# Performance work log

Hardware: AMD Instinct MI355X
Metric: run time of the kernel (lower is better)

## Reference

```python
import jax, jax.numpy as jnp
import numpy as np

B, H, W, C, NH, WS, SS = 16, 112, 112, 384, 12, 7, 3
HD = C // NH          # head dim = 32
N = WS * WS           # tokens per window = 49
MLP_H = 4 * C         # 1536
NW = (H // WS) * (W // WS)  # windows per image = 256


def _rel_pos_index():
    coords = np.stack(np.meshgrid(np.arange(WS), np.arange(WS), indexing='ij')).reshape(2, -1)
    rel = (coords[:, :, None] - coords[:, None, :]).transpose(1, 2, 0)  # (N, N, 2)
    rel[..., 0] += WS - 1
    rel[..., 1] += WS - 1
    rel[..., 0] *= 2 * WS - 1
    return rel.sum(-1)  # (N, N) in [0, (2WS-1)^2)


def _attn_mask():
    img = np.zeros((H, W))
    cnt = 0
    slices = (slice(0, -WS), slice(-WS, -SS), slice(-SS, None))
    for hs in slices:
        for ws_ in slices:
            img[hs, ws_] = cnt
            cnt += 1
    mw = img.reshape(H // WS, WS, W // WS, WS).transpose(0, 2, 1, 3).reshape(-1, N)
    am = mw[:, None, :] - mw[:, :, None]
    return np.where(am != 0, -100.0, 0.0).astype(np.float32)  # (NW, N, N)


REL_IDX = jnp.asarray(_rel_pos_index().reshape(-1))  # (N*N,) int
MASK = jnp.asarray(_attn_mask())                      # (NW, N, N)


def _ln(x, g, b, eps=1e-5):
    m = jnp.mean(x, -1, keepdims=True)
    v = jnp.mean((x - m) ** 2, -1, keepdims=True)
    return (x - m) / jnp.sqrt(v + eps) * g + b


def setup_inputs() -> dict:
    key = jax.random.key(0)
    ks = jax.random.split(key, 16)
    s = 0.02
    return {
        'x': jax.random.normal(ks[0], (B, H * W, C), jnp.float32),
        'norm1_g': jnp.ones((C,), jnp.float32),
        'norm1_b': jnp.zeros((C,), jnp.float32),
        'qkv_w': jax.random.normal(ks[1], (C, 3 * C), jnp.float32) * s,
        'qkv_b': jnp.zeros((3 * C,), jnp.float32),
        'proj_w': jax.random.normal(ks[2], (C, C), jnp.float32) * s,
        'proj_b': jnp.zeros((C,), jnp.float32),
        'rpb_table': jax.random.normal(ks[3], ((2 * WS - 1) ** 2, NH), jnp.float32) * s,
        'norm2_g': jnp.ones((C,), jnp.float32),
        'norm2_b': jnp.zeros((C,), jnp.float32),
        'fc1_w': jax.random.normal(ks[4], (C, MLP_H), jnp.float32) * s,
        'fc1_b': jnp.zeros((MLP_H,), jnp.float32),
        'fc2_w': jax.random.normal(ks[5], (MLP_H, C), jnp.float32) * s,
        'fc2_b': jnp.zeros((C,), jnp.float32),
    }


def reference(x, norm1_g, norm1_b, qkv_w, qkv_b, proj_w, proj_b, rpb_table,
              norm2_g, norm2_b, fc1_w, fc1_b, fc2_w, fc2_b):
    shortcut = x
    h = _ln(x, norm1_g, norm1_b).reshape(B, H, W, C)
    # cyclic shift
    h = jnp.roll(h, (-SS, -SS), axis=(1, 2))
    # window partition -> (B*NW, N, C)
    wins = h.reshape(B, H // WS, WS, W // WS, WS, C).transpose(0, 1, 3, 2, 4, 5).reshape(-1, N, C)
    qkv = (wins @ qkv_w + qkv_b).reshape(-1, N, 3, NH, HD).transpose(2, 0, 3, 1, 4)
    q, k, v = qkv[0] * HD ** -0.5, qkv[1], qkv[2]  # (B*NW, NH, N, HD)
    attn = jnp.einsum('bhnd,bhmd->bhnm', q, k)
    bias = rpb_table[REL_IDX].reshape(N, N, NH).transpose(2, 0, 1)  # (NH, N, N)
    attn = attn + bias[None]
    attn = (attn.reshape(B, NW, NH, N, N) + MASK[None, :, None]).reshape(-1, NH, N, N)
    attn = jax.nn.softmax(attn, axis=-1)
    out = jnp.einsum('bhnm,bhmd->bhnd', attn, v).transpose(0, 2, 1, 3).reshape(-1, N, C)
    out = out @ proj_w + proj_b
    # window reverse
    out = out.reshape(B, H // WS, W // WS, WS, WS, C).transpose(0, 1, 3, 2, 4, 5).reshape(B, H, W, C)
    out = jnp.roll(out, (SS, SS), axis=(1, 2)).reshape(B, H * W, C)
    x = shortcut + out
    h2 = _ln(x, norm2_g, norm2_b)
    h2 = jax.nn.gelu(h2 @ fc1_w + fc1_b, approximate=False) @ fc2_w + fc2_b
    return x + h2
```

## Files before the change

### kernel.cpp

```cpp
#include <hip/hip_runtime.h>
#include <hip/hip_bf16.h>

typedef short bf16x8 __attribute__((ext_vector_type(8)));
typedef float f32x4 __attribute__((ext_vector_type(4)));
typedef float f32x16 __attribute__((ext_vector_type(16)));
typedef unsigned int u32x4 __attribute__((ext_vector_type(4)));

typedef __attribute__((address_space(1))) void gvoid;
typedef __attribute__((address_space(3))) void lvoid;

__device__ __forceinline__ short f2b(float f) {
  __hip_bfloat16 h = __float2bfloat16(f);
  return __builtin_bit_cast(short, h);
}

__device__ __forceinline__ f32x4 mfma16(bf16x8 a, bf16x8 b, f32x4 c) {
  return __builtin_amdgcn_mfma_f32_16x16x32_bf16(a, b, c, 0, 0, 0);
}

__device__ __forceinline__ f32x16 mfma32(bf16x8 a, bf16x8 b, f32x16 c) {
  return __builtin_amdgcn_mfma_f32_32x32x16_bf16(a, b, c, 0, 0, 0);
}

__device__ __forceinline__ unsigned cvtpk(float lo, float hi) {
  unsigned r;
  asm("v_cvt_pk_bf16_f32 %0, %1, %2" : "=v"(r) : "v"(lo), "v"(hi));
  return r;
}

__device__ __forceinline__ void gload16(const void* g, void* l) {
  __builtin_amdgcn_global_load_lds((const gvoid*)g, (lvoid*)l, 16, 0, 0);
}

__global__ __launch_bounds__(256) void convT_k(const float* __restrict__ src,
                                               short* __restrict__ dst, int K,
                                               int N, int scale_cols,
                                               float scale) {
  int idx = blockIdx.x * 256 + threadIdx.x;
  if (idx >= N * K) return;
  int n = idx / K, k = idx % K;
  float v = src[(size_t)k * N + n];
  if (n < scale_cols) v *= scale;
  dst[idx] = f2b(v);
}

__global__ __launch_bounds__(256) void scale_bias_k(const float* __restrict__ src,
                                                    float* __restrict__ dst,
                                                    int n, int scale_cols,
                                                    float scale) {
  int i = blockIdx.x * 256 + threadIdx.x;
  if (i >= n) return;
  dst[i] = src[i] * (i < scale_cols ? scale : 1.f);
}

__global__ __launch_bounds__(256) void biasmask_k(const float* __restrict__ rpb,
                                                  float* __restrict__ tbl) {
  int idx = blockIdx.x * 256 + threadIdx.x;
  int q = idx & 63, key = (idx >> 6) & 63;
  int hc = idx >> 12;
  int h = hc % 12, cls = hc / 12;
  float v;
  if (q >= 49 || key >= 49) {
    v = -1e4f;
  } else {
    int i1 = q / 7, j1 = q % 7, i2 = key / 7, j2 = key % 7;
    v = rpb[(size_t)((i1 - i2 + 6) * 13 + (j1 - j2 + 6)) * 12 + h];
    int clsh = cls >> 1, clsw = cls & 1;
    int rq = (clsh ? 1 + (i1 >= 4) : 0) * 3 + (clsw ? 1 + (j1 >= 4) : 0);
    int rk = (clsh ? 1 + (i2 >= 4) : 0) * 3 + (clsw ? 1 + (j2 >= 4) : 0);
    if (rq != rk) v -= 100.f;
  }
  tbl[idx] = v;
}

template <bool GATHER>
__device__ __forceinline__ void ln_body(const float* __restrict__ x,
                                        const float* __restrict__ gw,
                                        const float* __restrict__ bw,
                                        short* __restrict__ out) {
  const int lane = threadIdx.x & 63;
  const int t = (blockIdx.x << 2) + (threadIdx.x >> 6);
  size_t srow;
  if (GATHER) {
    int bb = t / 12544, rm2 = t % 12544;
    int wi = rm2 / 49, nn = rm2 % 49;
    int wh = wi >> 4, ww = wi & 15;
    int ii = nn / 7, jj = nn % 7;
    int rr = wh * 7 + ii + 3; if (rr >= 112) rr -= 112;
    int cc = ww * 7 + jj + 3; if (cc >= 112) cc -= 112;
    srow = ((size_t)bb * 12544 + rr * 112 + cc) * 384;
  } else {
    srow = (size_t)t * 384;
  }
  const float2* src = (const float2*)(x + srow);
  const float2* g2 = (const float2*)gw;
  const float2* b2 = (const float2*)bw;
  float2 u[3];
  float s = 0.f, ss = 0.f;
#pragma unroll
  for (int k = 0; k < 3; ++k) {
    u[k] = src[lane + (k << 6)];
    s += u[k].x + u[k].y;
    ss += u[k].x * u[k].x + u[k].y * u[k].y;
  }
#pragma unroll
  for (int m = 1; m < 64; m <<= 1) {
    s += __shfl_xor(s, m, 64);
    ss += __shfl_xor(ss, m, 64);
  }
  const float mean = s * (1.f / 384.f);
  const float var = ss * (1.f / 384.f) - mean * mean;
  const float rstd = rsqrtf(var + 1e-5f);
  unsigned* o = (unsigned*)(out + (size_t)t * 384);
#pragma unroll
  for (int k = 0; k < 3; ++k) {
    int c = lane + (k << 6);
    float2 gv = g2[c], bv = b2[c];
    unsigned lo = (unsigned short)f2b((u[k].x - mean) * rstd * gv.x + bv.x);
    unsigned hi = (unsigned short)f2b((u[k].y - mean) * rstd * gv.y + bv.y);
    o[c] = lo | (hi << 16);
  }
}

__global__ __launch_bounds__(256) void ln1_k(const float* __restrict__ x,
                                             const float* __restrict__ gw,
                                             const float* __restrict__ bw,
                                             short* __restrict__ out) {
  ln_body<true>(x, gw, bw, out);
}
__global__ __launch_bounds__(256) void ln2_k(const float* __restrict__ x,
                                             const float* __restrict__ gw,
                                             const float* __restrict__ bw,
                                             short* __restrict__ out) {
  ln_body<false>(x, gw, bw, out);
}

template <int EPI>
__device__ __forceinline__ void gemm_body(
    const short* __restrict__ A, int lda, const short* __restrict__ BT,
    int ldb, const float* __restrict__ bias, int K, short* __restrict__ outh,
    int ldo, float* __restrict__ outf, const float* __restrict__ resid) {
  __shared__ __align__(16) short A0s[8192], B0s[8192];
  __shared__ __align__(16) short A1s[8192], B1s[8192];
  const int tid = threadIdx.x;
  const int gx = gridDim.x;
  int lin = blockIdx.y * gx + blockIdx.x;
  const int cpx = (gx * gridDim.y) >> 3;
  lin = (lin & 7) * cpx + (lin >> 3);
  const int m0 = (lin / gx) << 7, n0 = (lin % gx) << 7;
  const int lane = tid & 63;
  const int wave = tid >> 6;
  const int wr = (wave >> 1) << 6, wc = (wave & 1) << 6;
  const int g = lane >> 4, q = lane & 15;
  const int q7 = q & 7;
  const int rd0 = ((g) ^ q7) << 3;
  const int rd1 = ((4 + g) ^ q7) << 3;
  const int cswz = ((tid & 7) ^ ((tid >> 3) & 7)) << 3;
  const int ldst = tid << 3;

  f32x4 acc[4][4];
#pragma unroll
  for (int i = 0; i < 4; ++i)
#pragma unroll
    for (int j = 0; j < 4; ++j) acc[i][j] = (f32x4){0.f, 0.f, 0.f, 0.f};

  const short* Abase = A + (size_t)(m0 + (tid >> 3)) * lda + cswz;
  const short* Bbase = BT + (size_t)(n0 + (tid >> 3)) * ldb + cswz;

#define STAGE(kt, DA, DB)                                                     \
  do {                                                                        \
    _Pragma("unroll") for (int p = 0; p < 4; ++p) {                           \
      gload16(Abase + (size_t)(32 * p) * lda + (kt), &DA[2048 * p + ldst]);   \
      gload16(Bbase + (size_t)(32 * p) * ldb + (kt), &DB[2048 * p + ldst]);   \
    }                                                                         \
  } while (0)

#define COMPUTE(SA, SB)                                                       \
  do {                                                                        \
    _Pragma("unroll") for (int kk = 0; kk < 2; ++kk) {                        \
      const int rdo = kk ? rd1 : rd0;                                         \
      bf16x8 af[4], bfv[4];                                                   \
      _Pragma("unroll") for (int mi = 0; mi < 4; ++mi)                        \
          af[mi] = *(const bf16x8*)&SA[(wr + mi * 16 + q) * 64 + rdo];        \
      _Pragma("unroll") for (int ni = 0; ni < 4; ++ni)                        \
          bfv[ni] = *(const bf16x8*)&SB[(wc + ni * 16 + q) * 64 + rdo];       \
      _Pragma("unroll") for (int mi = 0; mi < 4; ++mi)                        \
          _Pragma("unroll") for (int ni = 0; ni < 4; ++ni)                    \
              acc[mi][ni] = mfma16(af[mi], bfv[ni], acc[mi][ni]);             \
    }                                                                         \
  } while (0)

  const int nt = K >> 6;
  STAGE(0, A0s, B0s);
  __syncthreads();
  for (int t = 0; t < nt; t += 2) {
    STAGE((t + 1) << 6, A1s, B1s);
    COMPUTE(A0s, B0s);
    __syncthreads();
    if (t + 2 < nt) STAGE((t + 2) << 6, A0s, B0s);
    COMPUTE(A1s, B1s);
    __syncthreads();
  }
#undef STAGE
#undef COMPUTE

  float bv[4];
#pragma unroll
  for (int ni = 0; ni < 4; ++ni)
    bv[ni] = bias ? bias[n0 + wc + ni * 16 + q] : 0.f;

#pragma unroll
  for (int mi = 0; mi < 4; ++mi) {
#pragma unroll
    for (int r = 0; r < 4; ++r) {
      const int grow = m0 + wr + mi * 16 + g * 4 + r;
      size_t orow;
      if constexpr (EPI == 2) {
        int bb = grow / 12544, rm2 = grow % 12544;
        int wi = rm2 / 49, nn = rm2 % 49;
        int wh = wi >> 4, ww = wi & 15;
        int ii = nn / 7, jj = nn % 7;
        int rr = wh * 7 + ii + 3; if (rr >= 112) rr -= 112;
        int cc = ww * 7 + jj + 3; if (cc >= 112) cc -= 112;
        orow = ((size_t)bb * 12544 + rr * 112 + cc) * 384;
      } else {
        orow = (size_t)grow * (size_t)ldo;
      }
#pragma unroll
      for (int ni = 0; ni < 4; ++ni) {
        const int gcol = n0 + wc + ni * 16 + q;
        float v = acc[mi][ni][r] + bv[ni];
        if constexpr (EPI == 0) {
          outh[orow + gcol] = f2b(v);
        } else if constexpr (EPI == 1) {
          v = 0.5f * v * (1.f + erff(v * 0.70710678118f));
          outh[orow + gcol] = f2b(v);
        } else if constexpr (EPI == 2) {
          outf[orow + gcol] = resid[orow + gcol] + v;
        } else {
          outf[orow + gcol] += v;
        }
      }
    }
  }
}

#define GEMM_WRAP(NAME, EPI)                                                   \
  __global__ __launch_bounds__(256) void NAME(                                 \
      const short* __restrict__ A, int lda, const short* __restrict__ BT,      \
      int ldb, const float* __restrict__ bias, int K,                          \
      short* __restrict__ outh, int ldo, float* __restrict__ outf,             \
      const float* __restrict__ resid) {                                       \
    gemm_body<EPI>(A, lda, BT, ldb, bias, K, outh, ldo, outf, resid);          \
  }
GEMM_WRAP(gemm_qkv_k, 0)
GEMM_WRAP(gemm_fc1_k, 1)
GEMM_WRAP(gemm_proj_k, 2)
GEMM_WRAP(gemm_fc2_k, 3)

__global__ __launch_bounds__(256) void attn_k(const short* __restrict__ qkv,
                                              const float* __restrict__ tbl,
                                              short* __restrict__ out) {
  const int lane = threadIdx.x & 63;
  const int task = blockIdx.x * 4 + (threadIdx.x >> 6);
  const int win = task / 12;
  const int h = task - win * 12;
  const int wh = (win >> 4) & 15, ww = win & 15;
  const int cls = ((wh == 15) ? 2 : 0) + ((ww == 15) ? 1 : 0);
  const int l31 = lane & 31, h5 = lane >> 5;
  const size_t tokbase = (size_t)win * 49;
  const short* base = qkv + tokbase * 1152 + h * 32;
  const bf16x8 zero8 = {0, 0, 0, 0, 0, 0, 0, 0};

  bf16x8 kf[2][2];
#pragma unroll
  for (int mi = 0; mi < 2; ++mi) {
    int row = l31 + 32 * mi;
#pragma unroll
    for (int s = 0; s < 2; ++s)
      kf[mi][s] = (row < 49)
                      ? *(const bf16x8*)(base + (size_t)row * 1152 + 384 +
                                         16 * s + 8 * h5)
                      : zero8;
  }
  bf16x8 vf[4];
#pragma unroll
  for (int kt = 0; kt < 4; ++kt) {
#pragma unroll
    for (int e = 0; e < 8; ++e) {
      int key = 16 * kt + 8 * h5 + e;
      vf[kt][e] = (key < 49) ? base[(size_t)key * 1152 + 768 + l31] : (short)0;
    }
  }

  const float* tb = tbl + ((size_t)(cls * 12 + h) << 12);

#pragma unroll
  for (int ni = 0; ni < 2; ++ni) {
    bf16x8 qf[2];
    int qrow = l31 + 32 * ni;
#pragma unroll
    for (int s = 0; s < 2; ++s)
      qf[s] = (qrow < 49)
                  ? *(const bf16x8*)(base + (size_t)qrow * 1152 + 16 * s +
                                     8 * h5)
                  : zero8;
    f32x16 st[2];
#pragma unroll
    for (int mi = 0; mi < 2; ++mi) {
      st[mi] = mfma32(kf[mi][0], qf[0], (f32x16)(0.f));
      st[mi] = mfma32(kf[mi][1], qf[1], st[mi]);
    }
#pragma unroll
    for (int mi = 0; mi < 2; ++mi)
#pragma unroll
      for (int r = 0; r < 16; ++r) {
        int koff = (r & 3) + 8 * (r >> 2) + 4 * h5;
        st[mi][r] += tb[(size_t)(32 * mi + koff) * 64 + 32 * ni + l31];
      }
    float mx = st[0][0];
#pragma unroll
    for (int r = 1; r < 16; ++r) mx = fmaxf(mx, st[0][r]);
#pragma unroll
    for (int r = 0; r < 16; ++r) mx = fmaxf(mx, st[1][r]);
    mx = fmaxf(mx, __shfl_xor(mx, 32, 64));
    float sm = 0.f;
#pragma unroll
    for (int mi = 0; mi < 2; ++mi)
#pragma unroll
      for (int r = 0; r < 16; ++r) {
        float e = __expf(st[mi][r] - mx);
        st[mi][r] = e;
        sm += e;
      }
    sm += __shfl_xor(sm, 32, 64);
    const float rinv = 1.f / sm;
#pragma unroll
    for (int mi = 0; mi < 2; ++mi)
#pragma unroll
      for (int r = 0; r < 16; ++r) st[mi][r] *= rinv;

    f32x16 acc = (f32x16)(0.f);
#pragma unroll
    for (int kt = 0; kt < 4; ++kt) {
      const int mi = kt >> 1, b8 = (kt & 1) * 8;
      unsigned q0l = cvtpk(st[mi][b8 + 0], st[mi][b8 + 1]);
      unsigned q0h = cvtpk(st[mi][b8 + 2], st[mi][b8 + 3]);
      unsigned q1l = cvtpk(st[mi][b8 + 4], st[mi][b8 + 5]);
      unsigned q1h = cvtpk(st[mi][b8 + 6], st[mi][b8 + 7]);
      unsigned sl = h5 ? q0l : q1l, sh = h5 ? q0h : q1h;
      unsigned kl = h5 ? q1l : q0l, kh = h5 ? q1h : q0h;
      unsigned rl = (unsigned)__shfl_xor((int)sl, 32, 64);
      unsigned rh = (unsigned)__shfl_xor((int)sh, 32, 64);
      u32x4 fr;
      fr[0] = h5 ? rl : kl;
      fr[1] = h5 ? rh : kh;
      fr[2] = h5 ? kl : rl;
      fr[3] = h5 ? kh : rh;
      acc = mfma32(__builtin_bit_cast(bf16x8, fr), vf[kt], acc);
    }
#pragma unroll
    for (int r = 0; r < 16; ++r) {
      int query = 32 * ni + (r & 3) + 8 * (r >> 2) + 4 * h5;
      if (ni == 0 || query < 49)
        out[(tokbase + query) * 384 + h * 32 + l31] = f2b(acc[r]);
    }
  }
}

extern "C" void kernel_launch(void* const* d_in, const int* in_sizes, int n_in,
                              void* d_out, int out_size, void* d_ws,
                              size_t ws_size, hipStream_t stream) {
  const float* x = (const float*)d_in[0];
  const float* n1g = (const float*)d_in[1];
  const float* n1b = (const float*)d_in[2];
  const float* qkvw = (const float*)d_in[3];
  const float* qkvb = (const float*)d_in[4];
  const float* projw = (const float*)d_in[5];
  const float* projb = (const float*)d_in[6];
  const float* rpb = (const float*)d_in[7];
  const float* n2g = (const float*)d_in[8];
  const float* n2b = (const float*)d_in[9];
  const float* fc1w = (const float*)d_in[10];
  const float* fc1b = (const float*)d_in[11];
  const float* fc2w = (const float*)d_in[12];
  const float* fc2b = (const float*)d_in[13];
  float* out = (float*)d_out;

  char* ws = (char*)d_ws;
  short* w_qkvT = (short*)(ws + 0);
  short* w_projT = (short*)(ws + 884736);
  short* w_fc1T = (short*)(ws + 1179648);
  short* w_fc2T = (short*)(ws + 2359296);
  float* w_qb = (float*)(ws + 3538944);
  float* tbl = (float*)(ws + 3543552);
  const size_t o_qkv = 4329984;
  short* qkvbuf = (short*)(ws + o_qkv);
  const size_t o_hwin = o_qkv + 462422016ull;
  short* hwin = (short*)(ws + o_hwin);
  const size_t o_fc1 = o_hwin + 154140672ull;

  int NC;
  size_t fc1_off = o_fc1;
  if (ws_size >= o_fc1 + 616562688ull) NC = 1;
  else if (ws_size >= o_fc1 + 308281344ull) NC = 2;
  else if (ws_size >= o_fc1 + 154140672ull) NC = 4;
  else { NC = 4; fc1_off = o_hwin; }
  short* fc1c = (short*)(ws + fc1_off);
  short* h2 = qkvbuf;

  const float qscale = 0.17677669529663687f;

  convT_k<<<(442368 + 255) / 256, 256, 0, stream>>>(qkvw, w_qkvT, 384, 1152, 384, qscale);
  convT_k<<<(147456 + 255) / 256, 256, 0, stream>>>(projw, w_projT, 384, 384, 0, 1.f);
  convT_k<<<(589824 + 255) / 256, 256, 0, stream>>>(fc1w, w_fc1T, 384, 1536, 0, 1.f);
  convT_k<<<(589824 + 255) / 256, 256, 0, stream>>>(fc2w, w_fc2T, 1536, 384, 0, 1.f);
  scale_bias_k<<<5, 256, 0, stream>>>(qkvb, w_qb, 1152, 384, qscale);
  biasmask_k<<<768, 256, 0, stream>>>(rpb, tbl);

  ln1_k<<<50176, 256, 0, stream>>>(x, n1g, n1b, hwin);
  gemm_qkv_k<<<dim3(9, 1568), 256, 0, stream>>>(hwin, 384, w_qkvT, 384, w_qb,
                                                384, qkvbuf, 1152, nullptr,
                                                nullptr);
  attn_k<<<12288, 256, 0, stream>>>(qkvbuf, tbl, hwin);
  gemm_proj_k<<<dim3(3, 1568), 256, 0, stream>>>(hwin, 384, w_projT, 384,
                                                 projb, 384, nullptr, 384, out,
                                                 x);
  ln2_k<<<50176, 256, 0, stream>>>(out, n2g, n2b, h2);
  const int CK = 1536 / NC;
  for (int c = 0; c < NC; ++c) {
    gemm_fc1_k<<<dim3(CK >> 7, 1568), 256, 0, stream>>>(
        h2, 384, w_fc1T + (size_t)c * CK * 384, 384, fc1b + c * CK, 384, fc1c,
        CK, nullptr, nullptr);
    gemm_fc2_k<<<dim3(3, 1568), 256, 0, stream>>>(
        fc1c, CK, w_fc2T + c * CK, 1536, (c == 0) ? fc2b : nullptr, CK,
        nullptr, 384, out, nullptr);
  }
}
```

Baseline: 2.128 ms.

## Interleave GEMM global-to-LDS loads with quadrant MFMA phases

Restructures the bf16 GEMM main loop into four quadrant MFMA phases per K-tile. Global-to-LDS loads for the next tile are split into halves and interleaved between the phases, with explicit vmcnt waits, raw s_barriers, and s_setprio raised around the MFMA bursts. The goal is to overlap memory traffic with matrix math and cut full-barrier stalls. This adds more barriers and hand-tuned wait counts, and the A01 load for tile t+2 is issued into the current buffer after its reads, so correctness depends on exact ordering.

```diff
diff --git a/kernel.cpp b/kernel.cpp
--- a/kernel.cpp
+++ b/kernel.cpp
@@ -167,42 +167,106 @@
   const short* Abase = A + (size_t)(m0 + (tid >> 3)) * lda + cswz;
   const short* Bbase = BT + (size_t)(n0 + (tid >> 3)) * ldb + cswz;
 
-#define STAGE(kt, DA, DB)                                                     \
-  do {                                                                        \
-    _Pragma("unroll") for (int p = 0; p < 4; ++p) {                           \
-      gload16(Abase + (size_t)(32 * p) * lda + (kt), &DA[2048 * p + ldst]);   \
-      gload16(Bbase + (size_t)(32 * p) * ldb + (kt), &DB[2048 * p + ldst]);   \
-    }                                                                         \
-  } while (0)
-
-#define COMPUTE(SA, SB)                                                       \
-  do {                                                                        \
-    _Pragma("unroll") for (int kk = 0; kk < 2; ++kk) {                        \
-      const int rdo = kk ? rd1 : rd0;                                         \
-      bf16x8 af[4], bfv[4];                                                   \
-      _Pragma("unroll") for (int mi = 0; mi < 4; ++mi)                        \
-          af[mi] = *(const bf16x8*)&SA[(wr + mi * 16 + q) * 64 + rdo];        \
-      _Pragma("unroll") for (int ni = 0; ni < 4; ++ni)                        \
-          bfv[ni] = *(const bf16x8*)&SB[(wc + ni * 16 + q) * 64 + rdo];       \
-      _Pragma("unroll") for (int mi = 0; mi < 4; ++mi)                        \
-          _Pragma("unroll") for (int ni = 0; ni < 4; ++ni)                    \
-              acc[mi][ni] = mfma16(af[mi], bfv[ni], acc[mi][ni]);             \
-    }                                                                         \
-  } while (0)
-
+#define SA01(kt, DA)                                            \
+  do {                                                          \
+    gload16(Abase + (kt), &DA[ldst]);                           \
+    gload16(Abase + (size_t)32 * lda + (kt), &DA[2048 + ldst]); \
+  } while (0)
+#define SA23(kt, DA)                                            \
+  do {                                                          \
+    gload16(Abase + (size_t)64 * lda + (kt), &DA[4096 + ldst]); \
+    gload16(Abase + (size_t)96 * lda + (kt), &DA[6144 + ldst]); \
+  } while (0)
+#define SB01(kt, DB)                                            \
+  do {                                                          \
+    gload16(Bbase + (kt), &DB[ldst]);                           \
+    gload16(Bbase + (size_t)32 * ldb + (kt), &DB[2048 + ldst]); \
+  } while (0)
+#define SB23(kt, DB)                                            \
+  do {                                                          \
+    gload16(Bbase + (size_t)64 * ldb + (kt), &DB[4096 + ldst]); \
+    gload16(Bbase + (size_t)96 * ldb + (kt), &DB[6144 + ldst]); \
+  } while (0)
+
+#define READ_AF(i, SA)                                               \
+  do {                                                               \
+    af[i][0] = *(const bf16x8*)&SA[(wr + (i)*16 + q) * 64 + rd0];    \
+    af[i][1] = *(const bf16x8*)&SA[(wr + (i)*16 + q) * 64 + rd1];    \
+  } while (0)
+#define READ_BF(i, SB)                                               \
+  do {                                                               \
+    bfr[i][0] = *(const bf16x8*)&SB[(wc + (i)*16 + q) * 64 + rd0];   \
+    bfr[i][1] = *(const bf16x8*)&SB[(wc + (i)*16 + q) * 64 + rd1];   \
+  } while (0)
+
+#define QUAD(a, b)                                                       \
+  do {                                                                   \
+    __builtin_amdgcn_s_setprio(1);                                       \
+    _Pragma("unroll") for (int ks = 0; ks < 2; ++ks)                     \
+        _Pragma("unroll") for (int i = 0; i < 2; ++i)                    \
+            _Pragma("unroll") for (int j = 0; j < 2; ++j)                \
+                acc[2 * (a) + i][2 * (b) + j] = mfma16(                  \
+                    af[2 * (a) + i][ks], bfr[2 * (b) + j][ks],           \
+                    acc[2 * (a) + i][2 * (b) + j]);                      \
+    __builtin_amdgcn_s_setprio(0);                                       \
+  } while (0)
+
+#define VMW2                                          \
+  do {                                                \
+    asm volatile("s_waitcnt vmcnt(2)" ::: "memory");  \
+    __builtin_amdgcn_sched_barrier(0);                \
+  } while (0)
+#define VMW0                                          \
+  do {                                                \
+    asm volatile("s_waitcnt vmcnt(0)" ::: "memory");  \
+    __builtin_amdgcn_sched_barrier(0);                \
+  } while (0)
+#define BAR __builtin_amdgcn_s_barrier()
+
+#define TILE(t, SA, SB, NA, NB)                              \
+  do {                                                       \
+    READ_AF(0, SA); READ_AF(1, SA);                          \
+    READ_BF(0, SB); READ_BF(1, SB);                          \
+    if ((t) + 1 < nt) SA23(((t) + 1) << 6, NA);              \
+    BAR; QUAD(0, 0); BAR;                                    \
+    READ_BF(2, SB); READ_BF(3, SB);                          \
+    if ((t) + 1 < nt) SB01(((t) + 1) << 6, NB);              \
+    BAR; QUAD(0, 1); BAR;                                    \
+    READ_AF(2, SA); READ_AF(3, SA);                          \
+    if ((t) + 1 < nt) SB23(((t) + 1) << 6, NB);              \
+    BAR; QUAD(1, 0); BAR;                                    \
+    __builtin_amdgcn_sched_barrier(0);                       \
+    if ((t) + 2 < nt) SA01(((t) + 2) << 6, SA);              \
+    QUAD(1, 1);                                              \
+    if ((t) + 1 < nt) {                                      \
+      if ((t) + 2 < nt) VMW2; else VMW0;                     \
+    }                                                        \
+    BAR;                                                     \
+  } while (0)
+
+  bf16x8 af[4][2], bfr[4][2];
   const int nt = K >> 6;
-  STAGE(0, A0s, B0s);
-  __syncthreads();
+
+  SA01(0, A0s); SA23(0, A0s); SB01(0, B0s); SB23(0, B0s);
+  SA01(64, A1s);
+  VMW2;
+  BAR;
+
   for (int t = 0; t < nt; t += 2) {
-    STAGE((t + 1) << 6, A1s, B1s);
-    COMPUTE(A0s, B0s);
-    __syncthreads();
-    if (t + 2 < nt) STAGE((t + 2) << 6, A0s, B0s);
-    COMPUTE(A1s, B1s);
-    __syncthreads();
-  }
-#undef STAGE
-#undef COMPUTE
+    TILE(t, A0s, B0s, A1s, B1s);
+    TILE(t + 1, A1s, B1s, A0s, B0s);
+  }
+#undef SA01
+#undef SA23
+#undef SB01
+#undef SB23
+#undef READ_AF
+#undef READ_BF
+#undef QUAD
+#undef VMW2
+#undef VMW0
+#undef BAR
+#undef TILE
 
   float bv[4];
 #pragma unroll
```

Result: no change. 2.100 ms (-1.3%).

## Use 8 waves per GEMM tile and swap MFMA operands for vectorized epilogue

Applied to the files above, without the earlier changes.

The 128x128 GEMM tile is now split across 8 waves (each 64x32) instead of 4 (each 64x64), and the block size goes to 512 threads. Each thread now issues half as many global-to-LDS loads per stage. The MFMA operands are swapped so each lane holds 4 consecutive output columns, which lets bias loads, bf16 stores and fp32 residual read-modify-writes use vector accesses instead of scalar ones. In exchange, each wave does less MFMA work per shared-memory fragment read, and it relies on ldo and the output columns being aligned to 4 elements.

```diff
diff --git a/kernel.cpp b/kernel.cpp
--- a/kernel.cpp
+++ b/kernel.cpp
@@ -5,6 +5,7 @@
 typedef float f32x4 __attribute__((ext_vector_type(4)));
 typedef float f32x16 __attribute__((ext_vector_type(16)));
 typedef unsigned int u32x4 __attribute__((ext_vector_type(4)));
+typedef unsigned int u32x2 __attribute__((ext_vector_type(2)));
 
 typedef __attribute__((address_space(1))) void gvoid;
 typedef __attribute__((address_space(3))) void lvoid;
@@ -150,7 +151,8 @@
   const int m0 = (lin / gx) << 7, n0 = (lin % gx) << 7;
   const int lane = tid & 63;
   const int wave = tid >> 6;
-  const int wr = (wave >> 1) << 6, wc = (wave & 1) << 6;
+  const int wr = (wave >> 2) << 6;
+  const int wc = (wave & 3) << 5;
   const int g = lane >> 4, q = lane & 15;
   const int q7 = q & 7;
   const int rd0 = ((g) ^ q7) << 3;
@@ -158,35 +160,35 @@
   const int cswz = ((tid & 7) ^ ((tid >> 3) & 7)) << 3;
   const int ldst = tid << 3;
 
-  f32x4 acc[4][4];
+  f32x4 acc[4][2];
 #pragma unroll
   for (int i = 0; i < 4; ++i)
 #pragma unroll
-    for (int j = 0; j < 4; ++j) acc[i][j] = (f32x4){0.f, 0.f, 0.f, 0.f};
+    for (int j = 0; j < 2; ++j) acc[i][j] = (f32x4){0.f, 0.f, 0.f, 0.f};
 
   const short* Abase = A + (size_t)(m0 + (tid >> 3)) * lda + cswz;
   const short* Bbase = BT + (size_t)(n0 + (tid >> 3)) * ldb + cswz;
 
-#define STAGE(kt, DA, DB)                                                     \
-  do {                                                                        \
-    _Pragma("unroll") for (int p = 0; p < 4; ++p) {                           \
-      gload16(Abase + (size_t)(32 * p) * lda + (kt), &DA[2048 * p + ldst]);   \
-      gload16(Bbase + (size_t)(32 * p) * ldb + (kt), &DB[2048 * p + ldst]);   \
-    }                                                                         \
+#define STAGE(kt, DA, DB)                                        \
+  do {                                                           \
+    gload16(Abase + (kt), &DA[ldst]);                            \
+    gload16(Abase + (size_t)64 * lda + (kt), &DA[4096 + ldst]);  \
+    gload16(Bbase + (kt), &DB[ldst]);                            \
+    gload16(Bbase + (size_t)64 * ldb + (kt), &DB[4096 + ldst]);  \
   } while (0)
 
 #define COMPUTE(SA, SB)                                                       \
   do {                                                                        \
     _Pragma("unroll") for (int kk = 0; kk < 2; ++kk) {                        \
       const int rdo = kk ? rd1 : rd0;                                         \
-      bf16x8 af[4], bfv[4];                                                   \
+      bf16x8 af[4], bfv[2];                                                   \
       _Pragma("unroll") for (int mi = 0; mi < 4; ++mi)                        \
           af[mi] = *(const bf16x8*)&SA[(wr + mi * 16 + q) * 64 + rdo];        \
-      _Pragma("unroll") for (int ni = 0; ni < 4; ++ni)                        \
+      _Pragma("unroll") for (int ni = 0; ni < 2; ++ni)                        \
           bfv[ni] = *(const bf16x8*)&SB[(wc + ni * 16 + q) * 64 + rdo];       \
       _Pragma("unroll") for (int mi = 0; mi < 4; ++mi)                        \
-          _Pragma("unroll") for (int ni = 0; ni < 4; ++ni)                    \
-              acc[mi][ni] = mfma16(af[mi], bfv[ni], acc[mi][ni]);             \
+          _Pragma("unroll") for (int ni = 0; ni < 2; ++ni)                    \
+              acc[mi][ni] = mfma16(bfv[ni], af[mi], acc[mi][ni]);             \
     }                                                                         \
   } while (0)
 
@@ -204,49 +206,59 @@
 #undef STAGE
 #undef COMPUTE
 
-  float bv[4];
-#pragma unroll
-  for (int ni = 0; ni < 4; ++ni)
-    bv[ni] = bias ? bias[n0 + wc + ni * 16 + q] : 0.f;
+  f32x4 bq[2];
+#pragma unroll
+  for (int ni = 0; ni < 2; ++ni)
+    bq[ni] = bias ? *(const f32x4*)&bias[n0 + wc + ni * 16 + g * 4]
+                  : (f32x4){0.f, 0.f, 0.f, 0.f};
 
 #pragma unroll
   for (int mi = 0; mi < 4; ++mi) {
-#pragma unroll
-    for (int r = 0; r < 4; ++r) {
-      const int grow = m0 + wr + mi * 16 + g * 4 + r;
-      size_t orow;
-      if constexpr (EPI == 2) {
-        int bb = grow / 12544, rm2 = grow % 12544;
-        int wi = rm2 / 49, nn = rm2 % 49;
-        int wh = wi >> 4, ww = wi & 15;
-        int ii = nn / 7, jj = nn % 7;
-        int rr = wh * 7 + ii + 3; if (rr >= 112) rr -= 112;
-        int cc = ww * 7 + jj + 3; if (cc >= 112) cc -= 112;
-        orow = ((size_t)bb * 12544 + rr * 112 + cc) * 384;
+    const int grow = m0 + wr + mi * 16 + q;
+    size_t orow;
+    if constexpr (EPI == 2) {
+      int bb = grow / 12544, rm2 = grow % 12544;
+      int wi = rm2 / 49, nn = rm2 % 49;
+      int wh = wi >> 4, ww = wi & 15;
+      int ii = nn / 7, jj = nn % 7;
+      int rr = wh * 7 + ii + 3; if (rr >= 112) rr -= 112;
+      int cc = ww * 7 + jj + 3; if (cc >= 112) cc -= 112;
+      orow = ((size_t)bb * 12544 + rr * 112 + cc) * 384;
+    } else {
+      orow = (size_t)grow * (size_t)ldo;
+    }
+#pragma unroll
+    for (int ni = 0; ni < 2; ++ni) {
+      const int gcol = n0 + wc + ni * 16 + g * 4;
+      float v[4];
+#pragma unroll
+      for (int j = 0; j < 4; ++j) v[j] = acc[mi][ni][j] + bq[ni][j];
+      if constexpr (EPI == 0) {
+        u32x2 u = {cvtpk(v[0], v[1]), cvtpk(v[2], v[3])};
+        *(u32x2*)&outh[orow + gcol] = u;
+      } else if constexpr (EPI == 1) {
+#pragma unroll
+        for (int j = 0; j < 4; ++j)
+          v[j] = 0.5f * v[j] * (1.f + erff(v[j] * 0.70710678118f));
+        u32x2 u = {cvtpk(v[0], v[1]), cvtpk(v[2], v[3])};
+        *(u32x2*)&outh[orow + gcol] = u;
+      } else if constexpr (EPI == 2) {
+        f32x4 r = *(const f32x4*)&resid[orow + gcol];
+#pragma unroll
+        for (int j = 0; j < 4; ++j) r[j] += v[j];
+        *(f32x4*)&outf[orow + gcol] = r;
       } else {
-        orow = (size_t)grow * (size_t)ldo;
+        f32x4 o = *(f32x4*)&outf[orow + gcol];
+#pragma unroll
+        for (int j = 0; j < 4; ++j) o[j] += v[j];
+        *(f32x4*)&outf[orow + gcol] = o;
       }
-#pragma unroll
-      for (int ni = 0; ni < 4; ++ni) {
-        const int gcol = n0 + wc + ni * 16 + q;
-        float v = acc[mi][ni][r] + bv[ni];
-        if constexpr (EPI == 0) {
-          outh[orow + gcol] = f2b(v);
-        } else if constexpr (EPI == 1) {
-          v = 0.5f * v * (1.f + erff(v * 0.70710678118f));
-          outh[orow + gcol] = f2b(v);
-        } else if constexpr (EPI == 2) {
-          outf[orow + gcol] = resid[orow + gcol] + v;
-        } else {
-          outf[orow + gcol] += v;
-        }
-      }
     }
   }
 }
 
 #define GEMM_WRAP(NAME, EPI)                                                   \
-  __global__ __launch_bounds__(256) void NAME(                                 \
+  __global__ __launch_bounds__(512) void NAME(                                 \
       const short* __restrict__ A, int lda, const short* __restrict__ BT,      \
       int ldb, const float* __restrict__ bias, int K,                          \
       short* __restrict__ outh, int ldo, float* __restrict__ outf,             \
@@ -419,20 +431,20 @@
   biasmask_k<<<768, 256, 0, stream>>>(rpb, tbl);
 
   ln1_k<<<50176, 256, 0, stream>>>(x, n1g, n1b, hwin);
-  gemm_qkv_k<<<dim3(9, 1568), 256, 0, stream>>>(hwin, 384, w_qkvT, 384, w_qb,
+  gemm_qkv_k<<<dim3(9, 1568), 512, 0, stream>>>(hwin, 384, w_qkvT, 384, w_qb,
                                                 384, qkvbuf, 1152, nullptr,
                                                 nullptr);
   attn_k<<<12288, 256, 0, stream>>>(qkvbuf, tbl, hwin);
-  gemm_proj_k<<<dim3(3, 1568), 256, 0, stream>>>(hwin, 384, w_projT, 384,
+  gemm_proj_k<<<dim3(3, 1568), 512, 0, stream>>>(hwin, 384, w_projT, 384,
                                                  projb, 384, nullptr, 384, out,
                                                  x);
   ln2_k<<<50176, 256, 0, stream>>>(out, n2g, n2b, h2);
   const int CK = 1536 / NC;
   for (int c = 0; c < NC; ++c) {
-    gemm_fc1_k<<<dim3(CK >> 7, 1568), 256, 0, stream>>>(
+    gemm_fc1_k<<<dim3(CK >> 7, 1568), 512, 0, stream>>>(
         h2, 384, w_fc1T + (size_t)c * CK * 384, 384, fc1b + c * CK, 384, fc1c,
         CK, nullptr, nullptr);
-    gemm_fc2_k<<<dim3(3, 1568), 256, 0, stream>>>(
+    gemm_fc2_k<<<dim3(3, 1568), 512, 0, stream>>>(
         fc1c, CK, w_fc2T + c * CK, 1536, (c == 0) ? fc2b : nullptr, CK,
         nullptr, 384, out, nullptr);
   }
```

Result: faster. 1.929 ms (-9.3%).
